# Performance work log

Measured on AMD Instinct MI355X. Metric: run time of the kernel, lower is better.

## Reference

```python
import jax, jax.numpy as jnp
import numpy as np

TEMP = 1.0  # routing_temperature

def _gelu(x):
    return jax.nn.gelu(x, approximate=False)  # torch nn.GELU default (erf)

def setup_inputs() -> dict:
    key = jax.random.key(0)
    ks = jax.random.split(key, 6)
    B, S, D, E, I = 8, 2048, 768, 8, 3072
    H = I // 2
    def xav(k, shape):
        fan_in, fan_out = shape[-2], shape[-1]
        lim = float(np.sqrt(6.0 / (fan_in + fan_out)))
        return jax.random.uniform(k, shape, jnp.float32, -lim, lim)
    return {
        "x":  jax.random.normal(ks[0], (B, S, D), jnp.float32),
        "Wr": xav(ks[1], (D, E)),
        "br": jnp.zeros((E,), jnp.float32),
        "W1": xav(ks[2], (E, D, I)), "b1": jnp.zeros((E, I), jnp.float32),
        "W2": xav(ks[3], (E, I, H)), "b2": jnp.zeros((E, H), jnp.float32),
        "W3": xav(ks[4], (E, H, D)), "b3": jnp.zeros((E, D), jnp.float32),
        "top_k": 2,
    }

def reference(x, Wr, br, W1, b1, W2, b2, W3, b3, top_k):
    B, S, D = x.shape
    E = Wr.shape[1]
    T = B * S
    xt = x.reshape(T, D)                              # flatten tokens
    logits = (xt @ Wr + br) / TEMP                    # [T, E]
    vals, sel = jax.lax.top_k(logits, top_k)          # [T, k]
    w = jax.nn.softmax(vals, axis=-1)                 # softmax over top-k scores
    # dense per-token combine weights (zero for unselected experts)
    combine = jnp.zeros((T, E), x.dtype).at[jnp.arange(T)[:, None], sel].add(w)
    def step(acc, p):
        W1e, b1e, W2e, b2e, W3e, b3e, ce = p
        h = _gelu(xt @ W1e + b1e)                     # [T, I]
        h = _gelu(h @ W2e + b2e)                      # [T, I//2]
        y = h @ W3e + b3e                             # [T, D]
        return acc + ce[:, None] * y, None
    acc0 = jnp.zeros((T, D), x.dtype)
    out, _ = jax.lax.scan(step, acc0, (W1, b1, W2, b2, W3, b3, combine.T))
    return out.reshape(B, S, D)
```

## Files before the change

kernel.cpp:

```cpp
#include <hip/hip_runtime.h>
#include <hip/hip_fp16.h>
#include <cstdint>
#include <cstddef>

#define TK 16384
#define DD 768
#define EE 8
#define II 3072
#define HH 1536

typedef _Float16 half8 __attribute__((ext_vector_type(8)));
typedef float floatx4 __attribute__((ext_vector_type(4)));

typedef const __attribute__((address_space(1))) uint32_t* gptr_t;
typedef __attribute__((address_space(3))) uint32_t* lptr_t;

#define GLOAD_LDS16(gp, lp) __builtin_amdgcn_global_load_lds( \
    (gptr_t)(const void*)(gp), (lptr_t)(void*)(lp), 16, 0, 0)

__global__ void cvt_kernel(const float* __restrict__ in, __half* __restrict__ out, long n) {
  long i = (long)blockIdx.x * blockDim.x + threadIdx.x;
  long stride = (long)gridDim.x * blockDim.x;
  for (long j = i * 4; j < n; j += stride * 4) {
    float4 v = *(const float4*)(in + j);
    __half2 a = __floats2half2_rn(v.x, v.y);
    __half2 b = __floats2half2_rn(v.z, v.w);
    uint2 p;
    p.x = *(const unsigned int*)&a;
    p.y = *(const unsigned int*)&b;
    *(uint2*)(out + j) = p;
  }
}

__global__ void cvtT_kernel(const float* __restrict__ in, __half* __restrict__ out,
                            int K, int N) {
  __shared__ float tile[32][33];
  int e = blockIdx.z;
  const float* inp = in + (size_t)e * K * N;
  __half* outp = out + (size_t)e * K * N;
  int n0 = blockIdx.x * 32, k0 = blockIdx.y * 32;
  int tx = threadIdx.x, ty = threadIdx.y;
#pragma unroll
  for (int i = 0; i < 4; ++i)
    tile[ty + i * 8][tx] = inp[(size_t)(k0 + ty + i * 8) * N + n0 + tx];
  __syncthreads();
#pragma unroll
  for (int i = 0; i < 4; ++i)
    outp[(size_t)(n0 + ty + i * 8) * K + k0 + tx] = __float2half(tile[tx][ty + i * 8]);
}

__global__ __launch_bounds__(256)
void router_kernel(const float* __restrict__ x, const float* __restrict__ Wr,
                   const float* __restrict__ br, int* __restrict__ counts,
                   int* __restrict__ sel, float* __restrict__ wTok) {
  __shared__ float wr_s[EE * DD];
  for (int i = threadIdx.x; i < EE * DD; i += 256) {
    int d = i >> 3, e = i & 7;
    wr_s[e * DD + d] = Wr[i];
  }
  __syncthreads();
  int wid = threadIdx.x >> 6, lane = threadIdx.x & 63;
  int t = blockIdx.x * 4 + wid;
  const float* xt = x + (size_t)t * DD;
  float acc[EE];
#pragma unroll
  for (int e = 0; e < EE; ++e) acc[e] = 0.f;
  for (int d = lane; d < DD; d += 64) {
    float xv = xt[d];
#pragma unroll
    for (int e = 0; e < EE; ++e) acc[e] += xv * wr_s[e * DD + d];
  }
#pragma unroll
  for (int off = 32; off > 0; off >>= 1)
#pragma unroll
    for (int e = 0; e < EE; ++e) acc[e] += __shfl_xor(acc[e], off);
  if (lane == 0) {
    float v[EE];
#pragma unroll
    for (int e = 0; e < EE; ++e) v[e] = acc[e] + br[e];
    int i0 = 0;
#pragma unroll
    for (int e = 1; e < EE; ++e) if (v[e] > v[i0]) i0 = e;
    int i1 = (i0 == 0) ? 1 : 0;
#pragma unroll
    for (int e = 0; e < EE; ++e) if (e != i0 && v[e] > v[i1] && e != i1) { if (v[e] > v[i1]) i1 = e; }
    float e1 = __expf(v[i1] - v[i0]);
    float s = 1.f / (1.f + e1);
    sel[2 * t] = i0; sel[2 * t + 1] = i1;
    wTok[2 * t] = s; wTok[2 * t + 1] = e1 * s;
    atomicAdd(&counts[i0], 1);
    atomicAdd(&counts[i1], 1);
  }
}

__global__ void offsets_kernel(const int* __restrict__ counts, int* __restrict__ offsets,
                               int* __restrict__ cursors) {
  if (threadIdx.x == 0) {
    int o = 0;
    for (int e = 0; e < EE; ++e) { offsets[e] = o; cursors[e] = o; o += counts[e]; }
  }
}

__global__ void scatter_kernel(const int* __restrict__ sel, int* __restrict__ cursors,
                               int* __restrict__ idxList, int* __restrict__ posTok) {
  int t = blockIdx.x * 256 + threadIdx.x;
  if (t < TK) {
#pragma unroll
    for (int k = 0; k < 2; ++k) {
      int e = sel[2 * t + k];
      int p = atomicAdd(&cursors[e], 1);
      idxList[p] = t;
      posTok[2 * t + k] = p;
    }
  }
}

template<int KD, int ND, bool GATHER, bool GELU>
__global__ __launch_bounds__(256)
void ffn_gemm(const __half* __restrict__ A, const __half* __restrict__ Wt,
              const float* __restrict__ Bias, __half* __restrict__ Out,
              const int* __restrict__ counts, const int* __restrict__ offsets,
              const int* __restrict__ idxList) {
  const int e = blockIdx.z;
  const int cnt = counts[e];
  const int m0 = blockIdx.y * 128;
  if (cnt == 0 || m0 >= cnt) return;
  const int off = offsets[e];
  const int n0 = blockIdx.x * 128;
  const __half* We = Wt + (size_t)e * KD * ND;
  const float* be = Bias + (size_t)e * ND;

  __shared__ __align__(16) __half As[128 * 64];
  __shared__ __align__(16) __half Bs[128 * 64];

  const int tid = threadIdx.x;

  const __half* abase[4];
  const __half* bbase[4];
#pragma unroll
  for (int i = 0; i < 4; ++i) {
    int s = i * 256 + tid;
    int row = s >> 3;
    int sc = s & 7;
    int r = m0 + row; if (r > cnt - 1) r = cnt - 1;
    size_t arow = GATHER ? (size_t)idxList[off + r] : (size_t)(off + r);
    abase[i] = A + arow * KD + ((sc ^ (row & 7)) << 3);
    bbase[i] = We + (size_t)(n0 + row) * KD + ((sc ^ (row & 7)) << 3);
  }

  floatx4 acc[4][4];
#pragma unroll
  for (int mi = 0; mi < 4; ++mi)
#pragma unroll
    for (int ni = 0; ni < 4; ++ni) acc[mi][ni] = (floatx4){0.f, 0.f, 0.f, 0.f};

  const int lane = tid & 63;
  const int wv = tid >> 6;
  const int wr = wv >> 1, wc = wv & 1;
  const int lrow = lane & 15, lg = lane >> 4;

  int aoff[4][2], boff[4][2];
#pragma unroll
  for (int mi = 0; mi < 4; ++mi) {
    int row = wr * 64 + mi * 16 + lrow;
#pragma unroll
    for (int kk = 0; kk < 2; ++kk) {
      int slot = kk * 4 + lg;
      aoff[mi][kk] = row * 64 + ((slot ^ (row & 7)) << 3);
    }
  }
#pragma unroll
  for (int ni = 0; ni < 4; ++ni) {
    int row = wc * 64 + ni * 16 + lrow;
#pragma unroll
    for (int kk = 0; kk < 2; ++kk) {
      int slot = kk * 4 + lg;
      boff[ni][kk] = row * 64 + ((slot ^ (row & 7)) << 3);
    }
  }

  for (int k0 = 0; k0 < KD; k0 += 64) {
    __syncthreads();
#pragma unroll
    for (int i = 0; i < 4; ++i)
      GLOAD_LDS16(abase[i] + k0, &As[i * 2048 + tid * 8]);
#pragma unroll
    for (int i = 0; i < 4; ++i)
      GLOAD_LDS16(bbase[i] + k0, &Bs[i * 2048 + tid * 8]);
    __syncthreads();
#pragma unroll
    for (int kk = 0; kk < 2; ++kk) {
      half8 af[4], bf[4];
#pragma unroll
      for (int mi = 0; mi < 4; ++mi) af[mi] = *(const half8*)&As[aoff[mi][kk]];
#pragma unroll
      for (int ni = 0; ni < 4; ++ni) bf[ni] = *(const half8*)&Bs[boff[ni][kk]];
#pragma unroll
      for (int mi = 0; mi < 4; ++mi)
#pragma unroll
        for (int ni = 0; ni < 4; ++ni)
          acc[mi][ni] = __builtin_amdgcn_mfma_f32_16x16x32_f16(af[mi], bf[ni], acc[mi][ni], 0, 0, 0);
    }
  }

#pragma unroll
  for (int ni = 0; ni < 4; ++ni) {
    int col = n0 + wc * 64 + ni * 16 + lrow;
    float bv = be[col];
#pragma unroll
    for (int mi = 0; mi < 4; ++mi) {
      int rbase = m0 + wr * 64 + mi * 16 + lg * 4;
#pragma unroll
      for (int j = 0; j < 4; ++j) {
        int r = rbase + j;
        if (r < cnt) {
          float v = acc[mi][ni][j] + bv;
          if (GELU) v = 0.5f * v * (1.f + erff(v * 0.70710678118654752f));
          Out[(size_t)(off + r) * ND + col] = __float2half(v);
        }
      }
    }
  }
}

__global__ void combine_kernel(const __half* __restrict__ yc, const float* __restrict__ wTok,
                               const int* __restrict__ posTok, float* __restrict__ out) {
  int t = blockIdx.x;
  int d = threadIdx.x * 4;
  if (d >= DD) return;
  float w0 = wTok[2 * t], w1 = wTok[2 * t + 1];
  const __half2* a = (const __half2*)(yc + (size_t)posTok[2 * t] * DD + d);
  const __half2* b = (const __half2*)(yc + (size_t)posTok[2 * t + 1] * DD + d);
  float2 a0 = __half22float2(a[0]), a1 = __half22float2(a[1]);
  float2 b0 = __half22float2(b[0]), b1 = __half22float2(b[1]);
  float4 r;
  r.x = w0 * a0.x + w1 * b0.x;
  r.y = w0 * a0.y + w1 * b0.y;
  r.z = w0 * a1.x + w1 * b1.x;
  r.w = w0 * a1.y + w1 * b1.y;
  *(float4*)(out + (size_t)t * DD + d) = r;
}

extern "C" void kernel_launch(void* const* d_in, const int* in_sizes, int n_in,
                              void* d_out, int out_size, void* d_ws, size_t ws_size,
                              hipStream_t stream) {
  const float* x  = (const float*)d_in[0];
  const float* Wr = (const float*)d_in[1];
  const float* br = (const float*)d_in[2];
  const float* W1 = (const float*)d_in[3];
  const float* b1 = (const float*)d_in[4];
  const float* W2 = (const float*)d_in[5];
  const float* b2 = (const float*)d_in[6];
  const float* W3 = (const float*)d_in[7];
  const float* b3 = (const float*)d_in[8];
  float* out = (float*)d_out;

  char* ws = (char*)d_ws;
  size_t o = 0;
  auto alloc = [&](size_t bytes) {
    char* p = ws + o;
    o += (bytes + 255) & ~(size_t)255;
    return p;
  };
  __half* xh   = (__half*)alloc((size_t)TK * DD * 2);
  __half* w1t  = (__half*)alloc((size_t)EE * DD * II * 2);
  __half* w2t  = (__half*)alloc((size_t)EE * II * HH * 2);
  __half* w3t  = (__half*)alloc((size_t)EE * HH * DD * 2);
  __half* h1   = (__half*)alloc((size_t)2 * TK * II * 2);
  __half* h2   = (__half*)alloc((size_t)2 * TK * HH * 2);
  __half* yc   = (__half*)alloc((size_t)2 * TK * DD * 2);
  int*   idxL  = (int*)alloc(2 * TK * 4);
  int*   sel   = (int*)alloc(2 * TK * 4);
  float* wTok  = (float*)alloc(2 * TK * 4);
  int*   posT  = (int*)alloc(2 * TK * 4);
  int*   counts  = (int*)alloc(256);
  int*   offsets = (int*)alloc(256);
  int*   cursors = (int*)alloc(256);
  if (o > ws_size) return;

  hipMemsetAsync(counts, 0, 256, stream);

  cvt_kernel<<<2048, 256, 0, stream>>>(x, xh, (long)TK * DD);
  cvtT_kernel<<<dim3(II / 32, DD / 32, EE), dim3(32, 8), 0, stream>>>(W1, w1t, DD, II);
  cvtT_kernel<<<dim3(HH / 32, II / 32, EE), dim3(32, 8), 0, stream>>>(W2, w2t, II, HH);
  cvtT_kernel<<<dim3(DD / 32, HH / 32, EE), dim3(32, 8), 0, stream>>>(W3, w3t, HH, DD);
  router_kernel<<<TK / 4, 256, 0, stream>>>(x, Wr, br, counts, sel, wTok);
  offsets_kernel<<<1, 64, 0, stream>>>(counts, offsets, cursors);
  scatter_kernel<<<TK / 256, 256, 0, stream>>>(sel, cursors, idxL, posT);

  ffn_gemm<DD, II, true, true><<<dim3(II / 128, 128, EE), 256, 0, stream>>>(
      xh, w1t, b1, h1, counts, offsets, idxL);
  ffn_gemm<II, HH, false, true><<<dim3(HH / 128, 128, EE), 256, 0, stream>>>(
      h1, w2t, b2, h2, counts, offsets, idxL);
  ffn_gemm<HH, DD, false, false><<<dim3(DD / 128, 128, EE), 256, 0, stream>>>(
      h2, w3t, b3, yc, counts, offsets, idxL);

  combine_kernel<<<TK, 192, 0, stream>>>(yc, wTok, posT, out);
}
```

Measured before the change: 1.746 ms.

## Rewrite MoE expert GEMM as 256x256 tile with double-buffered LDS pipeline

```diff
diff --git a/kernel.cpp b/kernel.cpp
--- a/kernel.cpp
+++ b/kernel.cpp
@@ -116,111 +116,144 @@
 }
 
 template<int KD, int ND, bool GATHER, bool GELU>
-__global__ __launch_bounds__(256)
+__global__ __launch_bounds__(512, 2)
 void ffn_gemm(const __half* __restrict__ A, const __half* __restrict__ Wt,
               const float* __restrict__ Bias, __half* __restrict__ Out,
               const int* __restrict__ counts, const int* __restrict__ offsets,
               const int* __restrict__ idxList) {
+  constexpr int NT = KD / 64;
   const int e = blockIdx.z;
   const int cnt = counts[e];
-  const int m0 = blockIdx.y * 128;
+  const int m0 = blockIdx.x * 256;
   if (cnt == 0 || m0 >= cnt) return;
   const int off = offsets[e];
-  const int n0 = blockIdx.x * 128;
+  const int n0 = blockIdx.y * 256;
   const __half* We = Wt + (size_t)e * KD * ND;
   const float* be = Bias + (size_t)e * ND;
 
-  __shared__ __align__(16) __half As[128 * 64];
-  __shared__ __align__(16) __half Bs[128 * 64];
+  __shared__ __align__(16) __half As[2][256 * 64];
+  __shared__ __align__(16) __half Bs[2][256 * 64];
 
   const int tid = threadIdx.x;
-
-  const __half* abase[4];
-  const __half* bbase[4];
-#pragma unroll
-  for (int i = 0; i < 4; ++i) {
-    int s = i * 256 + tid;
-    int row = s >> 3;
-    int sc = s & 7;
-    int r = m0 + row; if (r > cnt - 1) r = cnt - 1;
-    size_t arow = GATHER ? (size_t)idxList[off + r] : (size_t)(off + r);
-    abase[i] = A + arow * KD + ((sc ^ (row & 7)) << 3);
-    bbase[i] = We + (size_t)(n0 + row) * KD + ((sc ^ (row & 7)) << 3);
-  }
-
-  floatx4 acc[4][4];
-#pragma unroll
-  for (int mi = 0; mi < 4; ++mi)
+  const int srow = tid >> 3;
+  const int swz = ((tid & 7) ^ (srow & 7)) << 3;
+
+  const __half* aptr[4];
+  const __half* bptr[4];
+#pragma unroll
+  for (int q = 0; q < 4; ++q) {
+    int gr = m0 + q * 64 + srow;
+    if (gr > cnt - 1) gr = cnt - 1;
+    size_t arow = GATHER ? (size_t)idxList[off + gr] : (size_t)(off + gr);
+    aptr[q] = A + arow * KD + swz;
+    bptr[q] = We + (size_t)(n0 + q * 64 + srow) * KD + swz;
+  }
+
+#define STAGE_A(BUF, Q, TS) GLOAD_LDS16(aptr[Q] + (TS) * 64, &As[BUF][(Q) * 4096 + tid * 8])
+#define STAGE_B(BUF, Q, TS) GLOAD_LDS16(bptr[Q] + (TS) * 64, &Bs[BUF][(Q) * 4096 + tid * 8])
+
+  const int lane = tid & 63, wv = tid >> 6;
+  const int wr = wv >> 2, wc = wv & 3;
+  const int lrow = lane & 15, lg = lane >> 4;
+  const int rowa = wr * 128 + lrow;
+  const int rowb = wc * 64 + lrow;
+  int aoff[2], boff[2];
+#pragma unroll
+  for (int kk = 0; kk < 2; ++kk) {
+    aoff[kk] = rowa * 64 + (((kk * 4 + lg) ^ (rowa & 7)) << 3);
+    boff[kk] = rowb * 64 + (((kk * 4 + lg) ^ (rowb & 7)) << 3);
+  }
+
+  floatx4 acc[8][4];
+#pragma unroll
+  for (int mi = 0; mi < 8; ++mi)
 #pragma unroll
     for (int ni = 0; ni < 4; ++ni) acc[mi][ni] = (floatx4){0.f, 0.f, 0.f, 0.f};
 
-  const int lane = tid & 63;
-  const int wv = tid >> 6;
-  const int wr = wv >> 1, wc = wv & 1;
-  const int lrow = lane & 15, lg = lane >> 4;
-
-  int aoff[4][2], boff[4][2];
-#pragma unroll
-  for (int mi = 0; mi < 4; ++mi) {
-    int row = wr * 64 + mi * 16 + lrow;
-#pragma unroll
-    for (int kk = 0; kk < 2; ++kk) {
-      int slot = kk * 4 + lg;
-      aoff[mi][kk] = row * 64 + ((slot ^ (row & 7)) << 3);
-    }
-  }
-#pragma unroll
-  for (int ni = 0; ni < 4; ++ni) {
-    int row = wc * 64 + ni * 16 + lrow;
-#pragma unroll
-    for (int kk = 0; kk < 2; ++kk) {
-      int slot = kk * 4 + lg;
-      boff[ni][kk] = row * 64 + ((slot ^ (row & 7)) << 3);
-    }
-  }
-
-  for (int k0 = 0; k0 < KD; k0 += 64) {
-    __syncthreads();
-#pragma unroll
-    for (int i = 0; i < 4; ++i)
-      GLOAD_LDS16(abase[i] + k0, &As[i * 2048 + tid * 8]);
-#pragma unroll
-    for (int i = 0; i < 4; ++i)
-      GLOAD_LDS16(bbase[i] + k0, &Bs[i * 2048 + tid * 8]);
-    __syncthreads();
-#pragma unroll
-    for (int kk = 0; kk < 2; ++kk) {
-      half8 af[4], bf[4];
-#pragma unroll
-      for (int mi = 0; mi < 4; ++mi) af[mi] = *(const half8*)&As[aoff[mi][kk]];
-#pragma unroll
-      for (int ni = 0; ni < 4; ++ni) bf[ni] = *(const half8*)&Bs[boff[ni][kk]];
-#pragma unroll
-      for (int mi = 0; mi < 4; ++mi)
-#pragma unroll
-        for (int ni = 0; ni < 4; ++ni)
-          acc[mi][ni] = __builtin_amdgcn_mfma_f32_16x16x32_f16(af[mi], bf[ni], acc[mi][ni], 0, 0, 0);
-    }
-  }
-
-#pragma unroll
-  for (int ni = 0; ni < 4; ++ni) {
-    int col = n0 + wc * 64 + ni * 16 + lrow;
-    float bv = be[col];
-#pragma unroll
-    for (int mi = 0; mi < 4; ++mi) {
-      int rbase = m0 + wr * 64 + mi * 16 + lg * 4;
-#pragma unroll
-      for (int j = 0; j < 4; ++j) {
-        int r = rbase + j;
-        if (r < cnt) {
-          float v = acc[mi][ni][j] + bv;
+#pragma unroll
+  for (int q = 0; q < 4; ++q) STAGE_A(0, q, 0);
+#pragma unroll
+  for (int q = 0; q < 4; ++q) STAGE_B(0, q, 0);
+#pragma unroll
+  for (int q = 0; q < 4; ++q) STAGE_A(1, q, 1);
+  STAGE_B(1, 0, 1);
+  STAGE_B(1, 1, 1);
+  asm volatile("s_waitcnt vmcnt(6)" ::: "memory");
+  __builtin_amdgcn_s_barrier();
+
+#define BAR() __builtin_amdgcn_s_barrier()
+#define WLG() do { asm volatile("s_waitcnt lgkmcnt(0)" ::: "memory"); \
+                   __builtin_amdgcn_sched_barrier(0); } while (0)
+#define P1() __builtin_amdgcn_s_setprio(1)
+#define P0() __builtin_amdgcn_s_setprio(0)
+#define MMQ(AF, BF, MB, NB) \
+  _Pragma("unroll") for (int kk = 0; kk < 2; ++kk) \
+  _Pragma("unroll") for (int mi = 0; mi < 4; ++mi) \
+  _Pragma("unroll") for (int ni = 0; ni < 2; ++ni) \
+    acc[(MB) + mi][(NB) + ni] = __builtin_amdgcn_mfma_f32_16x16x32_f16( \
+        AF[mi][kk], BF[ni][kk], acc[(MB) + mi][(NB) + ni], 0, 0, 0);
+
+#define PHASES(CUR, NXT, TT) { \
+  const __half* Ac = &As[CUR][0]; \
+  const __half* Bc = &Bs[CUR][0]; \
+  half8 af[4][2], bf0[2][2], bf1[2][2]; \
+  _Pragma("unroll") for (int mi = 0; mi < 4; ++mi) \
+  _Pragma("unroll") for (int kk = 0; kk < 2; ++kk) \
+    af[mi][kk] = *(const half8*)&Ac[aoff[kk] + mi * 1024]; \
+  _Pragma("unroll") for (int ni = 0; ni < 2; ++ni) \
+  _Pragma("unroll") for (int kk = 0; kk < 2; ++kk) \
+    bf0[ni][kk] = *(const half8*)&Bc[boff[kk] + ni * 1024]; \
+  if ((TT) + 1 < NT) { STAGE_B(NXT, 2, (TT) + 1); STAGE_B(NXT, 3, (TT) + 1); } \
+  BAR(); WLG(); P1(); MMQ(af, bf0, 0, 0); P0(); BAR(); \
+  _Pragma("unroll") for (int ni = 0; ni < 2; ++ni) \
+  _Pragma("unroll") for (int kk = 0; kk < 2; ++kk) \
+    bf1[ni][kk] = *(const half8*)&Bc[boff[kk] + (ni + 2) * 1024]; \
+  if ((TT) + 2 < NT) { STAGE_A(CUR, 0, (TT) + 2); STAGE_A(CUR, 2, (TT) + 2); } \
+  BAR(); WLG(); P1(); MMQ(af, bf1, 0, 2); P0(); BAR(); \
+  _Pragma("unroll") for (int mi = 0; mi < 4; ++mi) \
+  _Pragma("unroll") for (int kk = 0; kk < 2; ++kk) \
+    af[mi][kk] = *(const half8*)&Ac[aoff[kk] + (mi + 4) * 1024]; \
+  if ((TT) + 2 < NT) { STAGE_B(CUR, 0, (TT) + 2); STAGE_B(CUR, 1, (TT) + 2); } \
+  BAR(); WLG(); P1(); MMQ(af, bf0, 4, 0); P0(); BAR(); \
+  if ((TT) + 2 < NT) { STAGE_A(CUR, 1, (TT) + 2); STAGE_A(CUR, 3, (TT) + 2); } \
+  BAR(); P1(); MMQ(af, bf1, 4, 2); P0(); \
+  if ((TT) + 2 < NT) { asm volatile("s_waitcnt vmcnt(6)" ::: "memory"); } \
+  else              { asm volatile("s_waitcnt vmcnt(0)" ::: "memory"); } \
+  BAR(); }
+
+  for (int t = 0; t < NT; t += 2) {
+    PHASES(0, 1, t)
+    PHASES(1, 0, t + 1)
+  }
+
+  const int crow = m0 + wr * 128 + lg * 4;
+  const int ccol = n0 + wc * 64 + lrow;
+  float bv[4];
+#pragma unroll
+  for (int ni = 0; ni < 4; ++ni) bv[ni] = be[ccol + ni * 16];
+#pragma unroll
+  for (int mi = 0; mi < 8; ++mi) {
+#pragma unroll
+    for (int j = 0; j < 4; ++j) {
+      int r = crow + mi * 16 + j;
+      if (r < cnt) {
+#pragma unroll
+        for (int ni = 0; ni < 4; ++ni) {
+          float v = acc[mi][ni][j] + bv[ni];
           if (GELU) v = 0.5f * v * (1.f + erff(v * 0.70710678118654752f));
-          Out[(size_t)(off + r) * ND + col] = __float2half(v);
+          Out[(size_t)(off + r) * ND + ccol + ni * 16] = __float2half(v);
         }
       }
     }
   }
+#undef STAGE_A
+#undef STAGE_B
+#undef BAR
+#undef WLG
+#undef P1
+#undef P0
+#undef MMQ
+#undef PHASES
 }
 
 __global__ void combine_kernel(const __half* __restrict__ yc, const float* __restrict__ wTok,
@@ -288,11 +321,11 @@
   offsets_kernel<<<1, 64, 0, stream>>>(counts, offsets, cursors);
   scatter_kernel<<<TK / 256, 256, 0, stream>>>(sel, cursors, idxL, posT);
 
-  ffn_gemm<DD, II, true, true><<<dim3(II / 128, 128, EE), 256, 0, stream>>>(
+  ffn_gemm<DD, II, true,  true ><<<dim3(64, II / 256, EE), 512, 0, stream>>>(
       xh, w1t, b1, h1, counts, offsets, idxL);
-  ffn_gemm<II, HH, false, true><<<dim3(HH / 128, 128, EE), 256, 0, stream>>>(
+  ffn_gemm<II, HH, false, true ><<<dim3(64, HH / 256, EE), 512, 0, stream>>>(
       h1, w2t, b2, h2, counts, offsets, idxL);
-  ffn_gemm<HH, DD, false, false><<<dim3(DD / 128, 128, EE), 256, 0, stream>>>(
+  ffn_gemm<HH, DD, false, false><<<dim3(64, DD / 256, EE), 512, 0, stream>>>(
       h2, w3t, b3, yc, counts, offsets, idxL);
 
   combine_kernel<<<TK, 192, 0, stream>>>(yc, wTok, posT, out);
```

After: 1.951 ms. +11.8%, slower.

## Double-buffer GEMM LDS tiles and fuse x fp16 conversion into router

Applied to the files above, without the earlier changes.

```diff
diff --git a/kernel.cpp b/kernel.cpp
--- a/kernel.cpp
+++ b/kernel.cpp
@@ -17,20 +17,6 @@
 
 #define GLOAD_LDS16(gp, lp) __builtin_amdgcn_global_load_lds( \
     (gptr_t)(const void*)(gp), (lptr_t)(void*)(lp), 16, 0, 0)
-
-__global__ void cvt_kernel(const float* __restrict__ in, __half* __restrict__ out, long n) {
-  long i = (long)blockIdx.x * blockDim.x + threadIdx.x;
-  long stride = (long)gridDim.x * blockDim.x;
-  for (long j = i * 4; j < n; j += stride * 4) {
-    float4 v = *(const float4*)(in + j);
-    __half2 a = __floats2half2_rn(v.x, v.y);
-    __half2 b = __floats2half2_rn(v.z, v.w);
-    uint2 p;
-    p.x = *(const unsigned int*)&a;
-    p.y = *(const unsigned int*)&b;
-    *(uint2*)(out + j) = p;
-  }
-}
 
 __global__ void cvtT_kernel(const float* __restrict__ in, __half* __restrict__ out,
                             int K, int N) {
@@ -52,7 +38,8 @@
 __global__ __launch_bounds__(256)
 void router_kernel(const float* __restrict__ x, const float* __restrict__ Wr,
                    const float* __restrict__ br, int* __restrict__ counts,
-                   int* __restrict__ sel, float* __restrict__ wTok) {
+                   int* __restrict__ sel, float* __restrict__ wTok,
+                   __half* __restrict__ xh) {
   __shared__ float wr_s[EE * DD];
   for (int i = threadIdx.x; i < EE * DD; i += 256) {
     int d = i >> 3, e = i & 7;
@@ -91,6 +78,18 @@
     atomicAdd(&counts[i0], 1);
     atomicAdd(&counts[i1], 1);
   }
+  const float4* xr = (const float4*)xt;
+  uint2* xo = (uint2*)(xh + (size_t)t * DD);
+#pragma unroll
+  for (int j = 0; j < 3; ++j) {
+    float4 v = xr[lane + j * 64];
+    __half2 a = __floats2half2_rn(v.x, v.y);
+    __half2 b = __floats2half2_rn(v.z, v.w);
+    uint2 p;
+    p.x = *(const unsigned int*)&a;
+    p.y = *(const unsigned int*)&b;
+    xo[lane + j * 64] = p;
+  }
 }
 
 __global__ void offsets_kernel(const int* __restrict__ counts, int* __restrict__ offsets,
@@ -116,11 +115,12 @@
 }
 
 template<int KD, int ND, bool GATHER, bool GELU>
-__global__ __launch_bounds__(256)
+__global__ __launch_bounds__(256, 2)
 void ffn_gemm(const __half* __restrict__ A, const __half* __restrict__ Wt,
               const float* __restrict__ Bias, __half* __restrict__ Out,
               const int* __restrict__ counts, const int* __restrict__ offsets,
               const int* __restrict__ idxList) {
+  constexpr int NT = KD / 64;
   const int e = blockIdx.z;
   const int cnt = counts[e];
   const int m0 = blockIdx.y * 128;
@@ -130,8 +130,8 @@
   const __half* We = Wt + (size_t)e * KD * ND;
   const float* be = Bias + (size_t)e * ND;
 
-  __shared__ __align__(16) __half As[128 * 64];
-  __shared__ __align__(16) __half Bs[128 * 64];
+  __shared__ __align__(16) __half As[2][128 * 64];
+  __shared__ __align__(16) __half Bs[2][128 * 64];
 
   const int tid = threadIdx.x;
 
@@ -179,29 +179,39 @@
     }
   }
 
-  for (int k0 = 0; k0 < KD; k0 += 64) {
-    __syncthreads();
-#pragma unroll
-    for (int i = 0; i < 4; ++i)
-      GLOAD_LDS16(abase[i] + k0, &As[i * 2048 + tid * 8]);
-#pragma unroll
-    for (int i = 0; i < 4; ++i)
-      GLOAD_LDS16(bbase[i] + k0, &Bs[i * 2048 + tid * 8]);
-    __syncthreads();
-#pragma unroll
-    for (int kk = 0; kk < 2; ++kk) {
-      half8 af[4], bf[4];
-#pragma unroll
-      for (int mi = 0; mi < 4; ++mi) af[mi] = *(const half8*)&As[aoff[mi][kk]];
-#pragma unroll
-      for (int ni = 0; ni < 4; ++ni) bf[ni] = *(const half8*)&Bs[boff[ni][kk]];
-#pragma unroll
-      for (int mi = 0; mi < 4; ++mi)
-#pragma unroll
-        for (int ni = 0; ni < 4; ++ni)
-          acc[mi][ni] = __builtin_amdgcn_mfma_f32_16x16x32_f16(af[mi], bf[ni], acc[mi][ni], 0, 0, 0);
-    }
-  }
+#pragma unroll
+  for (int i = 0; i < 4; ++i) GLOAD_LDS16(abase[i], &As[0][i * 2048 + tid * 8]);
+#pragma unroll
+  for (int i = 0; i < 4; ++i) GLOAD_LDS16(bbase[i], &Bs[0][i * 2048 + tid * 8]);
+  __syncthreads();
+
+#define TILE(CUR, NXT, TT)                                                    \
+  {                                                                           \
+    if ((TT) + 1 < NT) {                                                      \
+      _Pragma("unroll") for (int i = 0; i < 4; ++i)                           \
+        GLOAD_LDS16(abase[i] + ((TT) + 1) * 64, &As[NXT][i * 2048 + tid * 8]);\
+      _Pragma("unroll") for (int i = 0; i < 4; ++i)                           \
+        GLOAD_LDS16(bbase[i] + ((TT) + 1) * 64, &Bs[NXT][i * 2048 + tid * 8]);\
+    }                                                                         \
+    _Pragma("unroll") for (int kk = 0; kk < 2; ++kk) {                        \
+      half8 af[4], bf[4];                                                     \
+      _Pragma("unroll") for (int mi = 0; mi < 4; ++mi)                        \
+        af[mi] = *(const half8*)&As[CUR][aoff[mi][kk]];                       \
+      _Pragma("unroll") for (int ni = 0; ni < 4; ++ni)                        \
+        bf[ni] = *(const half8*)&Bs[CUR][boff[ni][kk]];                       \
+      _Pragma("unroll") for (int mi = 0; mi < 4; ++mi)                        \
+        _Pragma("unroll") for (int ni = 0; ni < 4; ++ni)                      \
+          acc[mi][ni] = __builtin_amdgcn_mfma_f32_16x16x32_f16(               \
+              af[mi], bf[ni], acc[mi][ni], 0, 0, 0);                          \
+    }                                                                         \
+    __syncthreads();   \
+  }
+
+  for (int t = 0; t < NT; t += 2) {
+    TILE(0, 1, t)
+    TILE(1, 0, t + 1)
+  }
+#undef TILE
 
 #pragma unroll
   for (int ni = 0; ni < 4; ++ni) {
@@ -280,17 +290,16 @@
 
   hipMemsetAsync(counts, 0, 256, stream);
 
-  cvt_kernel<<<2048, 256, 0, stream>>>(x, xh, (long)TK * DD);
   cvtT_kernel<<<dim3(II / 32, DD / 32, EE), dim3(32, 8), 0, stream>>>(W1, w1t, DD, II);
   cvtT_kernel<<<dim3(HH / 32, II / 32, EE), dim3(32, 8), 0, stream>>>(W2, w2t, II, HH);
   cvtT_kernel<<<dim3(DD / 32, HH / 32, EE), dim3(32, 8), 0, stream>>>(W3, w3t, HH, DD);
-  router_kernel<<<TK / 4, 256, 0, stream>>>(x, Wr, br, counts, sel, wTok);
+  router_kernel<<<TK / 4, 256, 0, stream>>>(x, Wr, br, counts, sel, wTok, xh);
   offsets_kernel<<<1, 64, 0, stream>>>(counts, offsets, cursors);
   scatter_kernel<<<TK / 256, 256, 0, stream>>>(sel, cursors, idxL, posT);
 
-  ffn_gemm<DD, II, true, true><<<dim3(II / 128, 128, EE), 256, 0, stream>>>(
+  ffn_gemm<DD, II, true,  true ><<<dim3(II / 128, 128, EE), 256, 0, stream>>>(
       xh, w1t, b1, h1, counts, offsets, idxL);
-  ffn_gemm<II, HH, false, true><<<dim3(HH / 128, 128, EE), 256, 0, stream>>>(
+  ffn_gemm<II, HH, false, true ><<<dim3(HH / 128, 128, EE), 256, 0, stream>>>(
       h1, w2t, b2, h2, counts, offsets, idxL);
   ffn_gemm<HH, DD, false, false><<<dim3(DD / 128, 128, EE), 256, 0, stream>>>(
       h2, w3t, b3, yc, counts, offsets, idxL);
```

Measured after the change: 1.687 ms. 1.03x faster.
